# Optimization experiments

Hardware: AMD Instinct MI355X
Metric: run time of the kernel (lower is better)

The kernel has to match this reference:

```python
import jax, jax.numpy as jnp
import numpy as np

K = 3
KK = K * K
PAD = 1          # kernel_size // 2
MAX_SHIFT = 8.0  # bias_range > 0
DEG = 2          # degrees = (2, 2), paon_type 'a'


def setup_inputs() -> dict:
    key = jax.random.key(0)
    ks = jax.random.split(key, 6)
    B, C, O, H, W = 4, 64, 64, 160, 160
    x = jax.random.normal(ks[0], (B, C, H, W), jnp.float32)
    # offset conv is 1x1: weight [2*K*K, C], bias [2*K*K]
    off_w = jax.random.normal(ks[1], (2 * KK, C), jnp.float32) * 0.1
    off_b = jax.random.normal(ks[2], (2 * KK,), jnp.float32) * 0.1
    scale = 1.0 / np.sqrt(C * KK).astype(np.float32)
    w_m = jax.random.normal(ks[3], (DEG * O, C, K, K), jnp.float32) * scale
    w_n = jax.random.normal(ks[4], (DEG * O, C, K, K), jnp.float32) * scale
    w0 = jax.random.normal(ks[5], (O,), jnp.float32) * 0.1
    return {"x": x, "off_w": off_w, "off_b": off_b, "w_m": w_m, "w_n": w_n, "w0": w0}


def _bilinear_sample(x, py, px):
    """x: [B,C,H,W]; py,px: [B,KK,H,W] -> [B,C,KK,H,W]; zero outside bounds."""
    B, C, H, W = x.shape
    xf = x.reshape(B, C, H * W)
    y0 = jnp.floor(py)
    x0 = jnp.floor(px)
    wy = py - y0
    wx = px - x0
    y0i = y0.astype(jnp.int32)
    x0i = x0.astype(jnp.int32)
    out = jnp.zeros((B, C) + py.shape[1:], x.dtype)
    corners = ((0, 0, (1 - wy) * (1 - wx)), (0, 1, (1 - wy) * wx),
               (1, 0, wy * (1 - wx)), (1, 1, wy * wx))
    for dy, dx, wgt in corners:
        yy = y0i + dy
        xx = x0i + dx
        valid = (yy >= 0) & (yy < H) & (xx >= 0) & (xx < W)
        idx = jnp.clip(yy, 0, H - 1) * W + jnp.clip(xx, 0, W - 1)
        g = jax.vmap(lambda f, i: f[:, i])(xf, idx.reshape(B, -1))  # [B,C,KK*H*W]
        out = out + g.reshape(B, C, *py.shape[1:]) * (wgt * valid)[:, None]
    return out


def _after_poly_a(y, ch, o, take_abs):
    # channel reorder + groupwise sum, per PaLaBase.after_poly_a
    order = np.array([(k * ch) % (ch * o) + k // o for k in range(ch * o)])
    y = y[:, order].reshape(y.shape[0], ch, o, *y.shape[2:])
    return jnp.abs(y).sum(2) if take_abs else y.sum(2)


def reference(x, off_w, off_b, w_m, w_n, w0):
    B, C, H, W = x.shape
    O = w0.shape[0]
    # --- DeformOffset: 1x1 conv -> clamp to image -> tanh soft-limit ---
    off_r = jnp.einsum('bchw,oc->bohw', x, off_w) + off_b[None, :, None, None]
    gy = jnp.arange(H, dtype=x.dtype)[None, None, :, None]
    gx = jnp.arange(W, dtype=x.dtype)[None, None, None, :]
    oy = jnp.clip(off_r[:, 0::2], -gy, H - gy)  # [B,KK,H,W] (dy per kernel pos)
    ox = jnp.clip(off_r[:, 1::2], -gx, W - gx)  # [B,KK,H,W] (dx per kernel pos)
    soft = lambda o: jnp.where(jnp.abs(o) >= MAX_SHIFT,
                               MAX_SHIFT * jnp.tanh(o / MAX_SHIFT), o)
    oy, ox = soft(oy), soft(ox)
    # --- deformable sampling grid (stride=1, dilation=1, zero padding) ---
    kidx = jnp.arange(KK)
    kh = (kidx // K).astype(x.dtype)[None, :, None, None]
    kw = (kidx % K).astype(x.dtype)[None, :, None, None]
    base_y = (jnp.arange(H, dtype=x.dtype) - PAD)[None, None, :, None]
    base_x = (jnp.arange(W, dtype=x.dtype) - PAD)[None, None, None, :]
    py = base_y + kh + oy
    px = base_x + kw + ox
    samp = _bilinear_sample(x, py, px)  # [B,C,KK,H,W]
    # --- Pade numerator / denominator convs on the sampled tensor ---
    pm_raw = jnp.einsum('bckhw,ock->bohw', samp, w_m.reshape(DEG * O, C, KK))
    qn_raw = jnp.einsum('bckhw,ock->bohw', samp, w_n.reshape(DEG * O, C, KK))
    pm = _after_poly_a(pm_raw, O, DEG, take_abs=False)
    qn = _after_poly_a(qn_raw, O, DEG, take_abs=True)
    # prepare_for_div_a: (pm + w0, 1 + qn)
    return (pm + w0[None, :, None, None]) / (1.0 + qn)
```

## Files before the change

### kernel.cpp

```cpp
#include <hip/hip_runtime.h>
#include <hip/hip_bf16.h>
#include <hip/hip_fp16.h>

#define Hh 160
#define Ww 160
#define Cc 64
#define HWc 25600
#define Bb 4
#define AST 76

typedef __attribute__((ext_vector_type(8))) _Float16 half8;
typedef __attribute__((ext_vector_type(4))) float f32x4;

__device__ __forceinline__ unsigned int f2h2u(float a, float b) {
  __half2 h = __floats2half2_rn(a, b);
  return *(unsigned int*)&h;
}

__global__ __launch_bounds__(256) void k_prep(
    const float* __restrict__ x, const float* __restrict__ wm,
    const float* __restrict__ wn, const float* __restrict__ ow,
    unsigned short* __restrict__ xT, unsigned short* __restrict__ bf) {
  if (blockIdx.x < 400) {
    __shared__ unsigned short s[64][260];
    int wg = blockIdx.x;
    int b = wg / 100;
    int pix0 = (wg % 100) * 256;
    int l = threadIdx.x & 63, wv = threadIdx.x >> 6;
    const float* xb = x + (size_t)b * Cc * HWc + pix0;
#pragma unroll
    for (int i = 0; i < 16; i++) {
      int c = i * 4 + wv;
      float4 v = *(const float4*)&xb[(size_t)c * HWc + l * 4];
      *(uint2*)&s[c][l * 4] = make_uint2(f2h2u(v.x, v.y), f2h2u(v.z, v.w));
    }
    __syncthreads();
    int p = threadIdx.x;
    unsigned int w[32];
#pragma unroll
    for (int j = 0; j < 32; j++) {
      unsigned int a = s[2 * j][p];
      unsigned int bb = s[2 * j + 1][p];
      w[j] = (a & 0xffffu) | (bb << 16);
    }
    unsigned short* dst = xT + ((size_t)(b * HWc + pix0 + p)) * 64;
#pragma unroll
    for (int j = 0; j < 8; j++)
      ((uint4*)dst)[j] = make_uint4(w[4 * j], w[4 * j + 1], w[4 * j + 2], w[4 * j + 3]);
  } else {
    int i = (blockIdx.x - 400) * 256 + threadIdx.x;
    if (i < 9 * 2 * 12 * 64 * 8) {
      int j2 = i & 7;
      int lane = (i >> 3) & 63;
      int ntck = i >> 9;
      int nt = ntck % 12;
      int ck = ntck / 12;
      int kk = ck >> 1;
      int chunk = ck & 1;
      int n = nt * 16 + (lane & 15);
      int c = chunk * 32 + (lane >> 4) * 8 + j2;
      float v;
      if (n < 64)
        v = wm[(n * 64 + c) * 9 + kk] + wm[((n + 64) * 64 + c) * 9 + kk];
      else
        v = wn[((n - 64) * 64 + c) * 9 + kk];
      __half hv = __float2half_rn(v);
      bf[i] = *(unsigned short*)&hv;
    } else if (i < 9 * 2 * 12 * 64 * 8 + 2 * 2 * 64 * 8) {
      int j = i - 9 * 2 * 12 * 64 * 8;
      int j2 = j & 7;
      int lane = (j >> 3) & 63;
      int rest = j >> 9;
      int ntile = rest & 1;
      int chunk = rest >> 1;
      int n = ntile * 16 + (lane & 15);
      int c = chunk * 32 + (lane >> 4) * 8 + j2;
      if (n < 18) {
        __half hv = __float2half_rn(ow[n * 64 + c]);
        bf[i] = *(unsigned short*)&hv;
      } else {
        bf[i] = 0;
      }
    }
  }
}

__device__ __forceinline__ void gather_issue(const char* __restrict__ gbase,
                                             uint4 D, int chB, uint4& c00,
                                             uint4& c01, uint4& c10,
                                             uint4& c11) {
  int bb = (int)D.x + chB;
  int dxB = (int)(D.y & 0xffffu);
  int dyB = (int)(D.y >> 16);
  c00 = *(const uint4*)(gbase + bb);
  c01 = *(const uint4*)(gbase + bb + dxB);
  c10 = *(const uint4*)(gbase + bb + dyB);
  c11 = *(const uint4*)(gbase + bb + dxB + dyB);
}

__device__ __forceinline__ void combine_write(unsigned short* Arow, uint4 D,
                                              const uint4& c00, const uint4& c01,
                                              const uint4& c10,
                                              const uint4& c11) {
  __half2 wz = *(const __half2*)&D.z;
  __half2 ww = *(const __half2*)&D.w;
  __half2 W00 = __half2half2(__low2half(wz));
  __half2 W01 = __half2half2(__high2half(wz));
  __half2 W10 = __half2half2(__low2half(ww));
  __half2 W11 = __half2half2(__high2half(ww));
  const unsigned int* a = (const unsigned int*)&c00;
  const unsigned int* b = (const unsigned int*)&c01;
  const unsigned int* c = (const unsigned int*)&c10;
  const unsigned int* d = (const unsigned int*)&c11;
  unsigned int o[4];
#pragma unroll
  for (int j = 0; j < 4; j++) {
    __half2 ha = *(const __half2*)&a[j];
    __half2 hb = *(const __half2*)&b[j];
    __half2 hc = *(const __half2*)&c[j];
    __half2 hd = *(const __half2*)&d[j];
    __half2 r = __hfma2(ha, W00,
                        __hfma2(hb, W01, __hfma2(hc, W10, __hmul2(hd, W11))));
    o[j] = *(unsigned int*)&r;
  }
  *(uint4*)Arow = make_uint4(o[0], o[1], o[2], o[3]);
}

__global__ __launch_bounds__(256, 4) void k_main(
    const unsigned short* __restrict__ xT, const float* __restrict__ w0,
    const float* __restrict__ off_b, const unsigned short* __restrict__ bfrag,
    const unsigned short* __restrict__ obfrag, float* __restrict__ out) {
  __shared__ unsigned short A[2][64 * AST];
  __shared__ uint4 gdesc[576];
  float2* spy = (float2*)&A[0][0];
  const int tid = threadIdx.x;
  const int wg = blockIdx.x;
  const int band = wg & 7;
  const int local = wg >> 3;
  const int b = local / 50;
  const int pix0 = band * 3200 + (local % 50) * 64;
  const int wv = tid >> 6;
  const int l = tid & 63;
  const int lm = l & 15;
  const int quad = l >> 4;
  const int ch8 = l & 7;
  const int pr = l >> 3;
  const int chB = ch8 * 16;
  const int pl0 = wv * 16 + pr;
  const int pl1 = wv * 16 + 8 + pr;

  const unsigned short* xTb = xT + (size_t)b * HWc * 64;
  const char* gbase = (const char*)xTb;

  f32x4 acc[3][4];
  const f32x4 zero = {0.f, 0.f, 0.f, 0.f};
#pragma unroll
  for (int j = 0; j < 3; j++)
#pragma unroll
    for (int pt = 0; pt < 4; pt++) acc[j][pt] = zero;

  {
    f32x4 aO0 = zero, aO1 = zero;
    const unsigned short* xrow = xTb + (size_t)(pix0 + wv * 16 + lm) * 64;
#pragma unroll
    for (int chunk = 0; chunk < 2; chunk++) {
      half8 sb = *(const half8*)(xrow + chunk * 32 + quad * 8);
      half8 wf0 = *(const half8*)&obfrag[((chunk * 2 + 0) * 64 + l) * 8];
      half8 wf1 = *(const half8*)&obfrag[((chunk * 2 + 1) * 64 + l) * 8];
      aO0 = __builtin_amdgcn_mfma_f32_16x16x32_f16(wf0, sb, aO0, 0, 0, 0);
      aO1 = __builtin_amdgcn_mfma_f32_16x16x32_f16(wf1, sb, aO1, 0, 0, 0);
    }
    int pix = pix0 + wv * 16 + lm;
    int h = pix / Ww, w = pix % Ww;
    float fh = (float)h, fw = (float)w;
#pragma unroll
    for (int rr = 0; rr < 2; rr++) {
      int n = quad * 4 + 2 * rr;
      int kk = n >> 1;
      float oy = aO0[2 * rr] + off_b[n];
      float ox = aO0[2 * rr + 1] + off_b[n + 1];
      oy = fminf(fmaxf(oy, -fh), 160.0f - fh);
      ox = fminf(fmaxf(ox, -fw), 160.0f - fw);
      if (fabsf(oy) >= 8.0f) oy = 8.0f * tanhf(oy * 0.125f);
      if (fabsf(ox) >= 8.0f) ox = 8.0f * tanhf(ox * 0.125f);
      spy[kk * 64 + wv * 16 + lm] =
          make_float2(fh - 1.0f + (float)(kk / 3) + oy,
                      fw - 1.0f + (float)(kk % 3) + ox);
    }
    if (quad == 0) {
      float oy = aO1[0] + off_b[16];
      float ox = aO1[1] + off_b[17];
      oy = fminf(fmaxf(oy, -fh), 160.0f - fh);
      ox = fminf(fmaxf(ox, -fw), 160.0f - fw);
      if (fabsf(oy) >= 8.0f) oy = 8.0f * tanhf(oy * 0.125f);
      if (fabsf(ox) >= 8.0f) ox = 8.0f * tanhf(ox * 0.125f);
      spy[8 * 64 + wv * 16 + lm] =
          make_float2(fh + 1.0f + oy, fw + 1.0f + ox);
    }
  }
  __syncthreads();

  for (int e = tid; e < 576; e += 256) {
    float2 P = spy[e];
    float py = P.x, pxv = P.y;
    float y0f = floorf(py), x0f = floorf(pxv);
    float wy = py - y0f, wx = pxv - x0f;
    int y0 = (int)y0f, x0 = (int)x0f;
    float vy0 = (y0 >= 0 && y0 < Hh) ? 1.f : 0.f;
    float vy1 = (y0 >= -1 && y0 < Hh - 1) ? 1.f : 0.f;
    float vx0 = (x0 >= 0 && x0 < Ww) ? 1.f : 0.f;
    float vx1 = (x0 >= -1 && x0 < Ww - 1) ? 1.f : 0.f;
    int r0 = min(max(y0, 0), Hh - 1);
    int r1 = min(max(y0 + 1, 0), Hh - 1);
    int c0 = min(max(x0, 0), Ww - 1);
    int c1 = min(max(x0 + 1, 0), Ww - 1);
    float w00 = (1.f - wy) * (1.f - wx) * vy0 * vx0;
    float w01 = (1.f - wy) * wx * vy0 * vx1;
    float w10 = wy * (1.f - wx) * vy1 * vx0;
    float w11 = wy * wx * vy1 * vx1;
    uint4 D;
    D.x = (unsigned int)((r0 * Ww + c0) * 128);
    D.y = (unsigned int)((c1 - c0) * 128) |
          ((unsigned int)((r1 - r0) * Ww * 128) << 16);
    D.z = f2h2u(w00, w01);
    D.w = f2h2u(w10, w11);
    gdesc[e] = D;
  }
  __syncthreads();

  half8 wf[2][2][3];
#pragma unroll
  for (int ch = 0; ch < 2; ch++)
#pragma unroll
    for (int j = 0; j < 3; j++) {
      int nt = j * 4 + wv;
      wf[0][ch][j] =
          *(const half8*)&bfrag[((size_t)(ch * 12 + nt) * 64 + l) * 8];
    }
  {
    uint4 D0 = gdesc[pl0], D1 = gdesc[pl1];
    uint4 a0, a1, a2, a3, b0, b1, b2, b3;
    gather_issue(gbase, D0, chB, a0, a1, a2, a3);
    gather_issue(gbase, D1, chB, b0, b1, b2, b3);
    combine_write(&A[0][pl0 * AST + ch8 * 8], D0, a0, a1, a2, a3);
    combine_write(&A[0][pl1 * AST + ch8 * 8], D1, b0, b1, b2, b3);
  }
  asm volatile("s_waitcnt lgkmcnt(0)" ::: "memory");
  __builtin_amdgcn_s_barrier();

#pragma unroll
  for (int kk = 0; kk < 9; kk++) {
    const int cur = kk & 1;
    const int sw = kk & 1;
    uint4 D0, D1;
    uint4 a0, a1, a2, a3, b0, b1, b2, b3;
    if (kk < 8) {
      D0 = gdesc[(kk + 1) * 64 + pl0];
      D1 = gdesc[(kk + 1) * 64 + pl1];
      gather_issue(gbase, D0, chB, a0, a1, a2, a3);
      gather_issue(gbase, D1, chB, b0, b1, b2, b3);
    }
#pragma unroll
    for (int chunk = 0; chunk < 2; chunk++) {
      half8 sfr[4];
#pragma unroll
      for (int pt = 0; pt < 4; pt++)
        sfr[pt] = *(const half8*)&A[cur][(pt * 16 + lm) * AST + chunk * 32 +
                                         quad * 8];
#pragma unroll
      for (int j = 0; j < 3; j++)
#pragma unroll
        for (int pt = 0; pt < 4; pt++)
          acc[j][pt] = __builtin_amdgcn_mfma_f32_16x16x32_f16(
              wf[sw][chunk][j], sfr[pt], acc[j][pt], 0, 0, 0);
      if (kk < 8) {
#pragma unroll
        for (int j = 0; j < 3; j++) {
          int nt = j * 4 + wv;
          wf[sw ^ 1][chunk][j] =
              *(const half8*)&bfrag[((size_t)(((kk + 1) * 2 + chunk) * 12 + nt) *
                                         64 + l) * 8];
        }
      }
    }
    if (kk < 8) {
      combine_write(&A[cur ^ 1][pl0 * AST + ch8 * 8], D0, a0, a1, a2, a3);
      combine_write(&A[cur ^ 1][pl1 * AST + ch8 * 8], D1, b0, b1, b2, b3);
      asm volatile("s_waitcnt lgkmcnt(0)" ::: "memory");
      __builtin_amdgcn_s_barrier();
    }
  }

  float w0v[4];
#pragma unroll
  for (int r = 0; r < 4; r++) w0v[r] = w0[wv * 16 + quad * 4 + r];
  float* ob = out + (size_t)b * Cc * HWc + pix0;
#pragma unroll
  for (int pt = 0; pt < 4; pt++) {
#pragma unroll
    for (int r = 0; r < 4; r++) {
      int oc = wv * 16 + quad * 4 + r;
      float pm = acc[0][pt][r] + w0v[r];
      float qn = 1.0f + fabsf(acc[1][pt][r]) + fabsf(acc[2][pt][r]);
      ob[oc * HWc + pt * 16 + lm] = pm / qn;
    }
  }
}

extern "C" void kernel_launch(void* const* d_in, const int* in_sizes, int n_in,
                              void* d_out, int out_size, void* d_ws, size_t ws_size,
                              hipStream_t stream) {
  const float* x = (const float*)d_in[0];
  const float* off_w = (const float*)d_in[1];
  const float* off_b = (const float*)d_in[2];
  const float* w_m = (const float*)d_in[3];
  const float* w_n = (const float*)d_in[4];
  const float* w0 = (const float*)d_in[5];
  float* out = (float*)d_out;

  unsigned short* bfrag = (unsigned short*)d_ws;
  unsigned short* obfrag = (unsigned short*)((char*)d_ws + (size_t)221184);
  unsigned short* xT = (unsigned short*)((char*)d_ws + (size_t)225280);

  hipLaunchKernelGGL(k_prep, dim3(840), dim3(256), 0, stream, x, w_m, w_n,
                     off_w, xT, bfrag);
  hipLaunchKernelGGL(k_main, dim3(1600), dim3(256), 0, stream, xT, w0, off_b,
                     bfrag, obfrag, out);
}
```

Measured before the change: 129.1 us.

## Deepen gather pipeline to two stages ahead with triple-buffered LDS

The bilinear gather loads are now issued two kernel positions ahead into two alternating register sets, and the LDS sample tile becomes triple-buffered, so global-load latency gets a full extra MFMA iteration to hide. Weight fragments are no longer double-buffered in registers; they are loaded right before use in each chunk, which frees registers for the extra gather set. The cost is more LDS per block, 32 live uint4 gather registers that may hurt occupancy at the 4-blocks launch bound, and weight-load latency that is now exposed just before the MFMAs.

```diff
diff --git a/kernel.cpp b/kernel.cpp
--- a/kernel.cpp
+++ b/kernel.cpp
@@ -98,12 +98,12 @@
   c11 = *(const uint4*)(gbase + bb + dxB + dyB);
 }
 
-__device__ __forceinline__ void combine_write(unsigned short* Arow, uint4 D,
+__device__ __forceinline__ void combine_write(unsigned short* Arow, uint2 Wzw,
                                               const uint4& c00, const uint4& c01,
                                               const uint4& c10,
                                               const uint4& c11) {
-  __half2 wz = *(const __half2*)&D.z;
-  __half2 ww = *(const __half2*)&D.w;
+  __half2 wz = *(const __half2*)&Wzw.x;
+  __half2 ww = *(const __half2*)&Wzw.y;
   __half2 W00 = __half2half2(__low2half(wz));
   __half2 W01 = __half2half2(__high2half(wz));
   __half2 W10 = __half2half2(__low2half(ww));
@@ -130,9 +130,10 @@
     const unsigned short* __restrict__ xT, const float* __restrict__ w0,
     const float* __restrict__ off_b, const unsigned short* __restrict__ bfrag,
     const unsigned short* __restrict__ obfrag, float* __restrict__ out) {
-  __shared__ unsigned short A[2][64 * AST];
+  __shared__ unsigned short A[3][64 * AST];
   __shared__ uint4 gdesc[576];
   float2* spy = (float2*)&A[0][0];
+  const uint2* gdw = (const uint2*)gdesc;
   const int tid = threadIdx.x;
   const int wg = blockIdx.x;
   const int band = wg & 7;
@@ -228,64 +229,70 @@
   }
   __syncthreads();
 
-  half8 wf[2][2][3];
-#pragma unroll
-  for (int ch = 0; ch < 2; ch++)
-#pragma unroll
-    for (int j = 0; j < 3; j++) {
-      int nt = j * 4 + wv;
-      wf[0][ch][j] =
-          *(const half8*)&bfrag[((size_t)(ch * 12 + nt) * 64 + l) * 8];
-    }
+  uint4 gA[8], gB[8];
   {
     uint4 D0 = gdesc[pl0], D1 = gdesc[pl1];
-    uint4 a0, a1, a2, a3, b0, b1, b2, b3;
-    gather_issue(gbase, D0, chB, a0, a1, a2, a3);
-    gather_issue(gbase, D1, chB, b0, b1, b2, b3);
-    combine_write(&A[0][pl0 * AST + ch8 * 8], D0, a0, a1, a2, a3);
-    combine_write(&A[0][pl1 * AST + ch8 * 8], D1, b0, b1, b2, b3);
+    gather_issue(gbase, D0, chB, gA[0], gA[1], gA[2], gA[3]);
+    gather_issue(gbase, D1, chB, gA[4], gA[5], gA[6], gA[7]);
+    uint4 E0 = gdesc[64 + pl0], E1 = gdesc[64 + pl1];
+    gather_issue(gbase, E0, chB, gB[0], gB[1], gB[2], gB[3]);
+    gather_issue(gbase, E1, chB, gB[4], gB[5], gB[6], gB[7]);
+    combine_write(&A[0][pl0 * AST + ch8 * 8], make_uint2(D0.z, D0.w), gA[0],
+                  gA[1], gA[2], gA[3]);
+    combine_write(&A[0][pl1 * AST + ch8 * 8], make_uint2(D1.z, D1.w), gA[4],
+                  gA[5], gA[6], gA[7]);
   }
   asm volatile("s_waitcnt lgkmcnt(0)" ::: "memory");
   __builtin_amdgcn_s_barrier();
 
 #pragma unroll
   for (int kk = 0; kk < 9; kk++) {
-    const int cur = kk & 1;
-    const int sw = kk & 1;
-    uint4 D0, D1;
-    uint4 a0, a1, a2, a3, b0, b1, b2, b3;
-    if (kk < 8) {
-      D0 = gdesc[(kk + 1) * 64 + pl0];
-      D1 = gdesc[(kk + 1) * 64 + pl1];
-      gather_issue(gbase, D0, chB, a0, a1, a2, a3);
-      gather_issue(gbase, D1, chB, b0, b1, b2, b3);
+    if (kk < 7) {
+      uint4 D0 = gdesc[(kk + 2) * 64 + pl0];
+      uint4 D1 = gdesc[(kk + 2) * 64 + pl1];
+      if ((kk & 1) == 0) {
+        gather_issue(gbase, D0, chB, gA[0], gA[1], gA[2], gA[3]);
+        gather_issue(gbase, D1, chB, gA[4], gA[5], gA[6], gA[7]);
+      } else {
+        gather_issue(gbase, D0, chB, gB[0], gB[1], gB[2], gB[3]);
+        gather_issue(gbase, D1, chB, gB[4], gB[5], gB[6], gB[7]);
+      }
     }
 #pragma unroll
     for (int chunk = 0; chunk < 2; chunk++) {
       half8 sfr[4];
 #pragma unroll
       for (int pt = 0; pt < 4; pt++)
-        sfr[pt] = *(const half8*)&A[cur][(pt * 16 + lm) * AST + chunk * 32 +
-                                         quad * 8];
+        sfr[pt] = *(const half8*)&A[kk % 3][(pt * 16 + lm) * AST + chunk * 32 +
+                                            quad * 8];
+      half8 wfr[3];
+#pragma unroll
+      for (int j = 0; j < 3; j++) {
+        int nt = j * 4 + wv;
+        wfr[j] = *(const half8*)&bfrag[((size_t)((kk * 2 + chunk) * 12 + nt) *
+                                           64 + l) * 8];
+      }
 #pragma unroll
       for (int j = 0; j < 3; j++)
 #pragma unroll
         for (int pt = 0; pt < 4; pt++)
           acc[j][pt] = __builtin_amdgcn_mfma_f32_16x16x32_f16(
-              wf[sw][chunk][j], sfr[pt], acc[j][pt], 0, 0, 0);
-      if (kk < 8) {
-#pragma unroll
-        for (int j = 0; j < 3; j++) {
-          int nt = j * 4 + wv;
-          wf[sw ^ 1][chunk][j] =
-              *(const half8*)&bfrag[((size_t)(((kk + 1) * 2 + chunk) * 12 + nt) *
-                                         64 + l) * 8];
-        }
+              wfr[j], sfr[pt], acc[j][pt], 0, 0, 0);
+    }
+    if (kk < 8) {
+      uint2 W0 = gdw[((kk + 1) * 64 + pl0) * 2 + 1];
+      uint2 W1 = gdw[((kk + 1) * 64 + pl1) * 2 + 1];
+      if (((kk + 1) & 1) == 0) {
+        combine_write(&A[(kk + 1) % 3][pl0 * AST + ch8 * 8], W0, gA[0], gA[1],
+                      gA[2], gA[3]);
+        combine_write(&A[(kk + 1) % 3][pl1 * AST + ch8 * 8], W1, gA[4], gA[5],
+                      gA[6], gA[7]);
+      } else {
+        combine_write(&A[(kk + 1) % 3][pl0 * AST + ch8 * 8], W0, gB[0], gB[1],
+                      gB[2], gB[3]);
+        combine_write(&A[(kk + 1) % 3][pl1 * AST + ch8 * 8], W1, gB[4], gB[5],
+                      gB[6], gB[7]);
       }
-    }
-    if (kk < 8) {
-      combine_write(&A[cur ^ 1][pl0 * AST + ch8 * 8], D0, a0, a1, a2, a3);
-      combine_write(&A[cur ^ 1][pl1 * AST + ch8 * 8], D1, b0, b1, b2, b3);
       asm volatile("s_waitcnt lgkmcnt(0)" ::: "memory");
       __builtin_amdgcn_s_barrier();
     }
```

New measurement: 143.3 us. +11.0%, slower.
